# Performance work log

Hardware: AMD Instinct MI355X
Metric: run time of the kernel (lower is better)

## Reference

```python
import jax, jax.numpy as jnp
import numpy as np

B, T, N, C, K = 32, 16, 512, 128, 2


def setup_inputs() -> dict:
    key = jax.random.key(0)
    k1, k2, k3 = jax.random.split(key, 3)
    x = jax.random.normal(k1, (B, T, N, C), dtype=jnp.float32)
    adj = jax.random.uniform(k2, (B, N, N), dtype=jnp.float32)
    lambdas = jnp.ones((K,), dtype=jnp.float32)           # raw lambda params (init 1.0)
    thetas = jax.random.uniform(k3, (K, C, C), dtype=jnp.float32)  # torch.rand init
    return {"x": x, "adj": adj, "lambdas": lambdas, "thetas": thetas}


def _akgcn_layer(x, adj, lam_raw, theta):
    # x: [B,T,N,C], adj: [B,N,N]
    lam = 1.0 + jax.nn.relu(lam_raw)  # actual lambda
    h = jnp.einsum('btnc,cd->btnd', x, theta)
    eye = jnp.eye(adj.shape[-1], dtype=adj.dtype)
    v = ((2.0 * lam - 2.0) / lam) * eye + (2.0 / lam) * adj   # [B,N,N]
    v = v / jnp.sum(v, axis=-1, keepdims=True)                 # row-normalize
    out = jnp.einsum('bnm,btmd->btnd', v, h)                   # vectorized over T
    return jax.nn.relu(out)


def reference(x, adj, lambdas, thetas):
    hid = x
    for k in range(K):  # small fixed layer count
        hid = _akgcn_layer(hid, adj, lambdas[k], thetas[k])
    return jax.nn.relu(x) + jax.nn.sigmoid(hid)
```

## Files before the change

kernel.cpp:

```cpp
#include <hip/hip_runtime.h>
#include <hip/hip_bf16.h>


typedef float f32x4 __attribute__((ext_vector_type(4)));
typedef __bf16 bf16x8 __attribute__((ext_vector_type(8)));

__device__ __forceinline__ unsigned short f2bf(float f) {
  union { float f; unsigned u; } v; v.f = f;
  unsigned r = v.u + 0x7FFFu + ((v.u >> 16) & 1u);
  return (unsigned short)(r >> 16);
}

__device__ __forceinline__ void gld16(const void* g, void* l) {
  __builtin_amdgcn_global_load_lds((const __attribute__((address_space(1))) void*)g,
                                   (__attribute__((address_space(3))) void*)l, 16, 0, 0);
}

__global__ __launch_bounds__(256) void akgcn_prep(
    const float* __restrict__ adj, const float* __restrict__ lambdas,
    const float* __restrict__ thetas, float* __restrict__ S,
    unsigned short* __restrict__ thT, unsigned short* __restrict__ adjk) {
  int bid = blockIdx.x;
  int tid = threadIdx.x;
  if (bid >= 16384) {
    int k = bid - 16384;
    const float* th = thetas + k * 16384;
    unsigned short* o = thT + k * 16384;
    for (int i = tid; i < 16384; i += 256) {
      int d = i >> 7, c = i & 127;
      o[i] = f2bf(th[c * 128 + d]);
    }
    return;
  }
  int n = bid & 511;
  float2 v = reinterpret_cast<const float2*>(adj + (size_t)bid * 512)[tid];
  float s = v.x + v.y;
#pragma unroll
  for (int off = 32; off > 0; off >>= 1) s += __shfl_down(s, off);
  __shared__ float red[4];
  if ((tid & 63) == 0) red[tid >> 6] = s;
  __syncthreads();
  if (tid == 0) S[bid] = red[0] + red[1] + red[2] + red[3];
  float dg0 = fmaxf(lambdas[0], 0.f);
  float dg1 = fmaxf(lambdas[1], 0.f);
  int m = tid * 2;
  ushort2 o0, o1;
  o0.x = f2bf(v.x + (m == n ? dg0 : 0.f));
  o0.y = f2bf(v.y + (m + 1 == n ? dg0 : 0.f));
  o1.x = f2bf(v.x + (m == n ? dg1 : 0.f));
  o1.y = f2bf(v.y + (m + 1 == n ? dg1 : 0.f));
  reinterpret_cast<ushort2*>(adjk + (size_t)bid * 512)[tid] = o0;
  reinterpret_cast<ushort2*>(adjk + 8388608ull + (size_t)bid * 512)[tid] = o1;
}

template <int LAYER>
__global__ __launch_bounds__(256) void akgcn_gemm1(
    const void* __restrict__ Ain, const unsigned short* __restrict__ thT,
    unsigned short* __restrict__ hT) {
  __shared__ unsigned short sm[32768];
  unsigned short* lA = sm;
  unsigned short* lB = sm + 16384;
  int bid = blockIdx.x;
  int tid = threadIdx.x;
  size_t r0 = (size_t)bid * 128;
  {
    const unsigned short* src = thT + LAYER * 16384;
#pragma unroll
    for (int it = 0; it < 8; ++it) {
      int idx = it * 2048 + tid * 8;
      uint4 u = *reinterpret_cast<const uint4*>(src + idx);
      int row = idx >> 7;
      unsigned byt = (unsigned)(idx * 2) ^ ((unsigned)(row & 15) << 4);
      *reinterpret_cast<uint4*>((char*)lB + byt) = u;
    }
  }
  if (LAYER == 0) {
    const float* A = (const float*)Ain + r0 * 128;
#pragma unroll
    for (int it = 0; it < 16; ++it) {
      int idx = it * 1024 + tid * 4;
      float4 f = *reinterpret_cast<const float4*>(A + idx);
      int row = idx >> 7;
      unsigned byt = (unsigned)(idx * 2) ^ ((unsigned)(row & 15) << 4);
      ushort4 u;
      u.x = f2bf(f.x); u.y = f2bf(f.y); u.z = f2bf(f.z); u.w = f2bf(f.w);
      *reinterpret_cast<ushort4*>((char*)lA + byt) = u;
    }
  } else {
    const unsigned short* A = (const unsigned short*)Ain + r0 * 128;
#pragma unroll
    for (int it = 0; it < 8; ++it) {
      int idx = it * 2048 + tid * 8;
      uint4 u = *reinterpret_cast<const uint4*>(A + idx);
      int row = idx >> 7;
      unsigned byt = (unsigned)(idx * 2) ^ ((unsigned)(row & 15) << 4);
      *reinterpret_cast<uint4*>((char*)lA + byt) = u;
    }
  }
  __syncthreads();
  int w = tid >> 6, wm = w >> 1, wn = w & 1;
  int lane = tid & 63, lr = lane & 15, lg = lane >> 4;
  f32x4 z = {0.f, 0.f, 0.f, 0.f};
  f32x4 acc[4][4];
#pragma unroll
  for (int mi = 0; mi < 4; ++mi)
#pragma unroll
    for (int ni = 0; ni < 4; ++ni) acc[mi][ni] = z;
#pragma unroll
  for (int ks = 0; ks < 4; ++ks) {
    bf16x8 av[4], bv[4];
#pragma unroll
    for (int mi = 0; mi < 4; ++mi) {
      int row = wm * 64 + mi * 16 + lr;
      unsigned byt = (unsigned)(row * 256 + ks * 64 + lg * 16) ^ ((unsigned)(row & 15) << 4);
      av[mi] = *reinterpret_cast<const bf16x8*>((const char*)lA + byt);
    }
#pragma unroll
    for (int ni = 0; ni < 4; ++ni) {
      int row = wn * 64 + ni * 16 + lr;
      unsigned byt = (unsigned)(row * 256 + ks * 64 + lg * 16) ^ ((unsigned)(row & 15) << 4);
      bv[ni] = *reinterpret_cast<const bf16x8*>((const char*)lB + byt);
    }
#pragma unroll
    for (int mi = 0; mi < 4; ++mi)
#pragma unroll
      for (int ni = 0; ni < 4; ++ni)
        acc[mi][ni] = __builtin_amdgcn_mfma_f32_16x16x32_bf16(av[mi], bv[ni], acc[mi][ni], 0, 0, 0);
  }
  __syncthreads();
#pragma unroll
  for (int mi = 0; mi < 4; ++mi) {
    int nloc = wm * 64 + mi * 16 + lg * 4;
#pragma unroll
    for (int ni = 0; ni < 4; ++ni) {
      int d = wn * 64 + ni * 16 + lr;
      ushort4 o;
      o.x = f2bf(acc[mi][ni][0]); o.y = f2bf(acc[mi][ni][1]);
      o.z = f2bf(acc[mi][ni][2]); o.w = f2bf(acc[mi][ni][3]);
      *reinterpret_cast<ushort4*>((char*)sm + d * 272 + nloc * 2) = o;
    }
  }
  __syncthreads();
  int bt = bid >> 2, n0 = (bid & 3) * 128;
#pragma unroll
  for (int i = 0; i < 8; ++i) {
    int c = i * 256 + tid;
    int dr = c >> 4, c8 = c & 15;
    uint4 u = *reinterpret_cast<const uint4*>((const char*)sm + dr * 272 + c8 * 16);
    *reinterpret_cast<uint4*>(hT + ((size_t)bt * 128 + dr) * 512 + n0 + c8 * 8) = u;
  }
}

template <int LAYER>
__global__ __launch_bounds__(256) void akgcn_gemm2(
    const unsigned short* __restrict__ adjm, const unsigned short* __restrict__ hT,
    const float* __restrict__ S, const float* __restrict__ lambdas,
    const float* __restrict__ x, void* __restrict__ outp) {
  __shared__ unsigned short ldsA[2][8192];
  __shared__ unsigned short ldsH[2][8192];
  __shared__ float inv[128];
  int tid = threadIdx.x;
  int wk = (blockIdx.x & 7) * 256 + (blockIdx.x >> 3);
  int b = wk >> 6, nb = (wk >> 4) & 3, t = wk & 15;
  int bt = b * 16 + t, n0 = nb * 128;
  float lam = 1.f + fmaxf(lambdas[LAYER], 0.f);
  float cc = 2.f / lam, aa = 2.f - cc;
  if (tid < 128) inv[tid] = cc / (aa + cc * S[b * 512 + n0 + tid]);
  const unsigned short* Abase = adjm + ((size_t)b * 512 + n0) * 512;
  const unsigned short* Hbase = hT + (size_t)bt * 65536;
  int w = tid >> 6, ln = tid & 63;
  int lr = ln & 15, lg = ln >> 4;
  int wm = w >> 1, wn = w & 1;
  int rsub = ln >> 3, c16 = ln & 7;

  auto stage = [&](int kt, int buf) {
    int m0 = kt * 64;
#pragma unroll
    for (int j = 0; j < 4; ++j) {
      int row = w * 32 + j * 8;
      gld16(Abase + (size_t)(row + rsub) * 512 + m0 + c16 * 8, &ldsA[buf][row * 64]);
      gld16(Hbase + (size_t)(row + rsub) * 512 + m0 + c16 * 8, &ldsH[buf][row * 64]);
    }
  };

  f32x4 z = {0.f, 0.f, 0.f, 0.f};
  f32x4 acc[4][4];
#pragma unroll
  for (int mi = 0; mi < 4; ++mi)
#pragma unroll
    for (int ni = 0; ni < 4; ++ni) acc[mi][ni] = z;

  stage(0, 0);
  __syncthreads();
  for (int kt = 0; kt < 8; ++kt) {
    int buf = kt & 1;
    if (kt < 7) stage(kt + 1, buf ^ 1);
#pragma unroll
    for (int ks = 0; ks < 2; ++ks) {
      bf16x8 av[4], bv[4];
#pragma unroll
      for (int mi = 0; mi < 4; ++mi) {
        int row = wm * 64 + mi * 16 + lr;
        av[mi] = *reinterpret_cast<const bf16x8*>((const char*)ldsH[buf] + row * 128 + ks * 64 + lg * 16);
      }
#pragma unroll
      for (int ni = 0; ni < 4; ++ni) {
        int row = wn * 64 + ni * 16 + lr;
        bv[ni] = *reinterpret_cast<const bf16x8*>((const char*)ldsA[buf] + row * 128 + ks * 64 + lg * 16);
      }
#pragma unroll
      for (int mi = 0; mi < 4; ++mi)
#pragma unroll
        for (int ni = 0; ni < 4; ++ni)
          acc[mi][ni] = __builtin_amdgcn_mfma_f32_16x16x32_bf16(av[mi], bv[ni], acc[mi][ni], 0, 0, 0);
    }
    __syncthreads();
  }

  size_t base_bt = (size_t)bt * 512;
#pragma unroll
  for (int ni = 0; ni < 4; ++ni) {
    int nl = wn * 64 + ni * 16 + lr;
    float iv = inv[nl];
    size_t rowbase = (base_bt + (size_t)(n0 + nl)) * 128;
#pragma unroll
    for (int mi = 0; mi < 4; ++mi) {
      int d0 = wm * 64 + mi * 16 + lg * 4;
      f32x4 a = acc[mi][ni];
      if (LAYER == 0) {
        ushort4 o;
        o.x = f2bf(fmaxf(a[0] * iv, 0.f)); o.y = f2bf(fmaxf(a[1] * iv, 0.f));
        o.z = f2bf(fmaxf(a[2] * iv, 0.f)); o.w = f2bf(fmaxf(a[3] * iv, 0.f));
        *reinterpret_cast<ushort4*>((unsigned short*)outp + rowbase + d0) = o;
      } else {
        float4 xv = *reinterpret_cast<const float4*>(x + rowbase + d0);
        float4 o;
        o.x = fmaxf(xv.x, 0.f) + 1.f / (1.f + __expf(-fmaxf(a[0] * iv, 0.f)));
        o.y = fmaxf(xv.y, 0.f) + 1.f / (1.f + __expf(-fmaxf(a[1] * iv, 0.f)));
        o.z = fmaxf(xv.z, 0.f) + 1.f / (1.f + __expf(-fmaxf(a[2] * iv, 0.f)));
        o.w = fmaxf(xv.w, 0.f) + 1.f / (1.f + __expf(-fmaxf(a[3] * iv, 0.f)));
        *reinterpret_cast<float4*>((float*)outp + rowbase + d0) = o;
      }
    }
  }
}

extern "C" void kernel_launch(void* const* d_in, const int* in_sizes, int n_in,
                              void* d_out, int out_size, void* d_ws, size_t ws_size,
                              hipStream_t stream) {
  const float* x = (const float*)d_in[0];
  const float* adj = (const float*)d_in[1];
  const float* lambdas = (const float*)d_in[2];
  const float* thetas = (const float*)d_in[3];
  char* ws = (char*)d_ws;
  float* S = (float*)ws;
  unsigned short* thT = (unsigned short*)(ws + 65536);
  unsigned short* adjk = (unsigned short*)(ws + 131072);
  unsigned short* hT = (unsigned short*)(ws + 131072 + 33554432);
  unsigned short* hid1 = (unsigned short*)d_out;

  akgcn_prep<<<16386, 256, 0, stream>>>(adj, lambdas, thetas, S, thT, adjk);
  akgcn_gemm1<0><<<2048, 256, 0, stream>>>((const void*)x, thT, hT);
  akgcn_gemm2<0><<<2048, 256, 0, stream>>>(adjk, hT, S, lambdas, nullptr, (void*)hid1);
  akgcn_gemm1<1><<<2048, 256, 0, stream>>>((const void*)hid1, thT, hT);
  akgcn_gemm2<1><<<2048, 256, 0, stream>>>(adjk + 8388608ull, hT, S, lambdas, x, d_out);
}
```

Before: 469.0 us.

## Fuse layer-2 feature GEMM into layer-1 aggregation epilogue and swizzle LDS

The layer-1 aggregation kernel now keeps its normalized, ReLU'd tile in LDS and multiplies it by the second theta right away, writing the transposed h for layer 2 directly. This removes one kernel launch and the global round-trip of the intermediate hidden tensor. The aggregation main loop also gains an XOR swizzle for LDS tiles to cut bank conflicts, and explicit vmcnt waits with raw barriers replace __syncthreads. The row-normalization factors are now loaded straight into registers. The cost is extra LDS reuse, higher register pressure from a second accumulator set, and a heavier epilogue in layer 0.

After: 430.4 us. 8.2% less time.

```diff
diff --git a/kernel.cpp b/kernel.cpp
--- a/kernel.cpp
+++ b/kernel.cpp
@@ -53,9 +53,8 @@
   reinterpret_cast<ushort2*>(adjk + 8388608ull + (size_t)bid * 512)[tid] = o1;
 }
 
-template <int LAYER>
 __global__ __launch_bounds__(256) void akgcn_gemm1(
-    const void* __restrict__ Ain, const unsigned short* __restrict__ thT,
+    const float* __restrict__ x, const unsigned short* __restrict__ thT,
     unsigned short* __restrict__ hT) {
   __shared__ unsigned short sm[32768];
   unsigned short* lA = sm;
@@ -64,18 +63,17 @@
   int tid = threadIdx.x;
   size_t r0 = (size_t)bid * 128;
   {
-    const unsigned short* src = thT + LAYER * 16384;
 #pragma unroll
     for (int it = 0; it < 8; ++it) {
       int idx = it * 2048 + tid * 8;
-      uint4 u = *reinterpret_cast<const uint4*>(src + idx);
+      uint4 u = *reinterpret_cast<const uint4*>(thT + idx);
       int row = idx >> 7;
       unsigned byt = (unsigned)(idx * 2) ^ ((unsigned)(row & 15) << 4);
       *reinterpret_cast<uint4*>((char*)lB + byt) = u;
     }
   }
-  if (LAYER == 0) {
-    const float* A = (const float*)Ain + r0 * 128;
+  {
+    const float* A = x + r0 * 128;
 #pragma unroll
     for (int it = 0; it < 16; ++it) {
       int idx = it * 1024 + tid * 4;
@@ -86,16 +84,6 @@
       u.x = f2bf(f.x); u.y = f2bf(f.y); u.z = f2bf(f.z); u.w = f2bf(f.w);
       *reinterpret_cast<ushort4*>((char*)lA + byt) = u;
     }
-  } else {
-    const unsigned short* A = (const unsigned short*)Ain + r0 * 128;
-#pragma unroll
-    for (int it = 0; it < 8; ++it) {
-      int idx = it * 2048 + tid * 8;
-      uint4 u = *reinterpret_cast<const uint4*>(A + idx);
-      int row = idx >> 7;
-      unsigned byt = (unsigned)(idx * 2) ^ ((unsigned)(row & 15) << 4);
-      *reinterpret_cast<uint4*>((char*)lA + byt) = u;
-    }
   }
   __syncthreads();
   int w = tid >> 6, wm = w >> 1, wn = w & 1;
@@ -155,17 +143,16 @@
 __global__ __launch_bounds__(256) void akgcn_gemm2(
     const unsigned short* __restrict__ adjm, const unsigned short* __restrict__ hT,
     const float* __restrict__ S, const float* __restrict__ lambdas,
-    const float* __restrict__ x, void* __restrict__ outp) {
+    const float* __restrict__ x, const unsigned short* __restrict__ thT1,
+    void* __restrict__ outp) {
   __shared__ unsigned short ldsA[2][8192];
   __shared__ unsigned short ldsH[2][8192];
-  __shared__ float inv[128];
   int tid = threadIdx.x;
   int wk = (blockIdx.x & 7) * 256 + (blockIdx.x >> 3);
   int b = wk >> 6, nb = (wk >> 4) & 3, t = wk & 15;
   int bt = b * 16 + t, n0 = nb * 128;
   float lam = 1.f + fmaxf(lambdas[LAYER], 0.f);
   float cc = 2.f / lam, aa = 2.f - cc;
-  if (tid < 128) inv[tid] = cc / (aa + cc * S[b * 512 + n0 + tid]);
   const unsigned short* Abase = adjm + ((size_t)b * 512 + n0) * 512;
   const unsigned short* Hbase = hT + (size_t)bt * 65536;
   int w = tid >> 6, ln = tid & 63;
@@ -175,11 +162,12 @@
 
   auto stage = [&](int kt, int buf) {
     int m0 = kt * 64;
+    int scol = m0 + ((c16 ^ rsub) << 3);
 #pragma unroll
     for (int j = 0; j < 4; ++j) {
-      int row = w * 32 + j * 8;
-      gld16(Abase + (size_t)(row + rsub) * 512 + m0 + c16 * 8, &ldsA[buf][row * 64]);
-      gld16(Hbase + (size_t)(row + rsub) * 512 + m0 + c16 * 8, &ldsH[buf][row * 64]);
+      int rowb = w * 32 + j * 8;
+      gld16(Abase + (size_t)(rowb + rsub) * 512 + scol, &ldsA[buf][rowb * 64]);
+      gld16(Hbase + (size_t)(rowb + rsub) * 512 + scol, &ldsH[buf][rowb * 64]);
     }
   };
 
@@ -191,22 +179,29 @@
     for (int ni = 0; ni < 4; ++ni) acc[mi][ni] = z;
 
   stage(0, 0);
-  __syncthreads();
   for (int kt = 0; kt < 8; ++kt) {
     int buf = kt & 1;
-    if (kt < 7) stage(kt + 1, buf ^ 1);
+    if (kt < 7) {
+      stage(kt + 1, buf ^ 1);
+      asm volatile("s_waitcnt vmcnt(8)" ::: "memory");
+    } else {
+      asm volatile("s_waitcnt vmcnt(0)" ::: "memory");
+    }
+    __builtin_amdgcn_s_barrier();
 #pragma unroll
     for (int ks = 0; ks < 2; ++ks) {
       bf16x8 av[4], bv[4];
 #pragma unroll
       for (int mi = 0; mi < 4; ++mi) {
         int row = wm * 64 + mi * 16 + lr;
-        av[mi] = *reinterpret_cast<const bf16x8*>((const char*)ldsH[buf] + row * 128 + ks * 64 + lg * 16);
+        unsigned byt = (unsigned)(row * 128 + ks * 64 + lg * 16) ^ ((unsigned)(row & 7) << 4);
+        av[mi] = *reinterpret_cast<const bf16x8*>((const char*)ldsH[buf] + byt);
       }
 #pragma unroll
       for (int ni = 0; ni < 4; ++ni) {
         int row = wn * 64 + ni * 16 + lr;
-        bv[ni] = *reinterpret_cast<const bf16x8*>((const char*)ldsA[buf] + row * 128 + ks * 64 + lg * 16);
+        unsigned byt = (unsigned)(row * 128 + ks * 64 + lg * 16) ^ ((unsigned)(row & 7) << 4);
+        bv[ni] = *reinterpret_cast<const bf16x8*>((const char*)ldsA[buf] + byt);
       }
 #pragma unroll
       for (int mi = 0; mi < 4; ++mi)
@@ -214,25 +209,90 @@
         for (int ni = 0; ni < 4; ++ni)
           acc[mi][ni] = __builtin_amdgcn_mfma_f32_16x16x32_bf16(av[mi], bv[ni], acc[mi][ni], 0, 0, 0);
     }
-    __syncthreads();
-  }
-
-  size_t base_bt = (size_t)bt * 512;
-#pragma unroll
-  for (int ni = 0; ni < 4; ++ni) {
-    int nl = wn * 64 + ni * 16 + lr;
-    float iv = inv[nl];
-    size_t rowbase = (base_bt + (size_t)(n0 + nl)) * 128;
-#pragma unroll
-    for (int mi = 0; mi < 4; ++mi) {
-      int d0 = wm * 64 + mi * 16 + lg * 4;
-      f32x4 a = acc[mi][ni];
-      if (LAYER == 0) {
+    __builtin_amdgcn_s_barrier();
+  }
+
+  float invv[4];
+#pragma unroll
+  for (int ni = 0; ni < 4; ++ni)
+    invv[ni] = cc / (aa + cc * S[b * 512 + n0 + wn * 64 + ni * 16 + lr]);
+
+  if (LAYER == 0) {
+    unsigned short* hidT = &ldsA[0][0];
+    unsigned short* thL = &ldsH[0][0];
+#pragma unroll
+    for (int ni = 0; ni < 4; ++ni) {
+      int n = wn * 64 + ni * 16 + lr;
+      float iv = invv[ni];
+#pragma unroll
+      for (int mi = 0; mi < 4; ++mi) {
+        int d0 = wm * 64 + mi * 16 + lg * 4;
+        f32x4 a = acc[mi][ni];
         ushort4 o;
         o.x = f2bf(fmaxf(a[0] * iv, 0.f)); o.y = f2bf(fmaxf(a[1] * iv, 0.f));
         o.z = f2bf(fmaxf(a[2] * iv, 0.f)); o.w = f2bf(fmaxf(a[3] * iv, 0.f));
-        *reinterpret_cast<ushort4*>((unsigned short*)outp + rowbase + d0) = o;
-      } else {
+        unsigned byt = (unsigned)(n * 256 + d0 * 2) ^ ((unsigned)(n & 15) << 4);
+        *reinterpret_cast<ushort4*>((char*)hidT + byt) = o;
+      }
+    }
+#pragma unroll
+    for (int j = 0; j < 8; ++j) {
+      int rowb = w * 32 + j * 4;
+      int row = rowb + (ln >> 4);
+      int c = ln & 15;
+      gld16(thT1 + (size_t)row * 128 + ((c ^ (row & 15)) << 3), &thL[rowb * 128]);
+    }
+    __syncthreads();
+    f32x4 acc2[4][4];
+#pragma unroll
+    for (int mi = 0; mi < 4; ++mi)
+#pragma unroll
+      for (int ni = 0; ni < 4; ++ni) acc2[mi][ni] = z;
+#pragma unroll
+    for (int ks = 0; ks < 4; ++ks) {
+      bf16x8 av[4], bv[4];
+#pragma unroll
+      for (int mi = 0; mi < 4; ++mi) {
+        int n = wm * 64 + mi * 16 + lr;
+        unsigned byt = (unsigned)(n * 256 + ks * 64 + lg * 16) ^ ((unsigned)(n & 15) << 4);
+        av[mi] = *reinterpret_cast<const bf16x8*>((const char*)hidT + byt);
+      }
+#pragma unroll
+      for (int ni = 0; ni < 4; ++ni) {
+        int e = wn * 64 + ni * 16 + lr;
+        unsigned byt = (unsigned)(e * 256 + ks * 64 + lg * 16) ^ ((unsigned)(e & 15) << 4);
+        bv[ni] = *reinterpret_cast<const bf16x8*>((const char*)thL + byt);
+      }
+#pragma unroll
+      for (int mi = 0; mi < 4; ++mi)
+#pragma unroll
+        for (int ni = 0; ni < 4; ++ni)
+          acc2[mi][ni] = __builtin_amdgcn_mfma_f32_16x16x32_bf16(av[mi], bv[ni], acc2[mi][ni], 0, 0, 0);
+    }
+    unsigned short* hT2 = (unsigned short*)outp;
+#pragma unroll
+    for (int ni = 0; ni < 4; ++ni) {
+      int e = wn * 64 + ni * 16 + lr;
+      unsigned short* dst = hT2 + ((size_t)bt * 128 + e) * 512 + n0;
+#pragma unroll
+      for (int mi = 0; mi < 4; ++mi) {
+        int nn = wm * 64 + mi * 16 + lg * 4;
+        f32x4 a = acc2[mi][ni];
+        ushort4 o;
+        o.x = f2bf(a[0]); o.y = f2bf(a[1]); o.z = f2bf(a[2]); o.w = f2bf(a[3]);
+        *reinterpret_cast<ushort4*>(dst + nn) = o;
+      }
+    }
+  } else {
+#pragma unroll
+    for (int ni = 0; ni < 4; ++ni) {
+      int nl = wn * 64 + ni * 16 + lr;
+      float iv = invv[ni];
+      size_t rowbase = ((size_t)bt * 512 + (size_t)(n0 + nl)) * 128;
+#pragma unroll
+      for (int mi = 0; mi < 4; ++mi) {
+        int d0 = wm * 64 + mi * 16 + lg * 4;
+        f32x4 a = acc[mi][ni];
         float4 xv = *reinterpret_cast<const float4*>(x + rowbase + d0);
         float4 o;
         o.x = fmaxf(xv.x, 0.f) + 1.f / (1.f + __expf(-fmaxf(a[0] * iv, 0.f)));
@@ -256,12 +316,10 @@
   float* S = (float*)ws;
   unsigned short* thT = (unsigned short*)(ws + 65536);
   unsigned short* adjk = (unsigned short*)(ws + 131072);
-  unsigned short* hT = (unsigned short*)(ws + 131072 + 33554432);
-  unsigned short* hid1 = (unsigned short*)d_out;
-
+  unsigned short* hT2 = (unsigned short*)(ws + 131072 + 33554432);
+  unsigned short* hTd = (unsigned short*)d_out;
   akgcn_prep<<<16386, 256, 0, stream>>>(adj, lambdas, thetas, S, thT, adjk);
-  akgcn_gemm1<0><<<2048, 256, 0, stream>>>((const void*)x, thT, hT);
-  akgcn_gemm2<0><<<2048, 256, 0, stream>>>(adjk, hT, S, lambdas, nullptr, (void*)hid1);
-  akgcn_gemm1<1><<<2048, 256, 0, stream>>>((const void*)hid1, thT, hT);
-  akgcn_gemm2<1><<<2048, 256, 0, stream>>>(adjk + 8388608ull, hT, S, lambdas, x, d_out);
-}
+  akgcn_gemm1<<<2048, 256, 0, stream>>>(x, thT, hTd);
+  akgcn_gemm2<0><<<2048, 256, 0, stream>>>(adjk, hTd, S, lambdas, nullptr, thT + 16384, hT2);
+  akgcn_gemm2<1><<<2048, 256, 0, stream>>>(adjk + 8388608ull, hT2, S, lambdas, x, nullptr, d_out);
+}
```
